# Kernel optimization log

Measured on AMD Instinct MI355X. Metric: run time of the kernel, lower is better.

## Reference

```python
import jax, jax.numpy as jnp
import numpy as np

N_NODES = 50000
HEADS = 4
NEG_SLOPE = 0.2


def _gat_conv(x, src, dst, W, a_src, a_dst, b):
    """PyG GATConv (concat=True, add_self_loops already applied to src/dst).
    x: [N, F_in], W: [F_in, H*C], a_src/a_dst: [H, C], b: [H*C]."""
    N = x.shape[0]
    HC = W.shape[1]
    C = HC // HEADS
    h = (x @ W).reshape(N, HEADS, C)                       # [N, H, C]
    alpha_s = (h * a_src[None]).sum(-1)                    # [N, H]
    alpha_d = (h * a_dst[None]).sum(-1)                    # [N, H]
    e = jax.nn.leaky_relu(alpha_s[src] + alpha_d[dst], NEG_SLOPE)  # [E, H]
    # segment softmax over incoming edges of each destination node
    m = jax.ops.segment_max(e, dst, num_segments=N)        # [N, H]
    ex = jnp.exp(e - m[dst])
    denom = jax.ops.segment_sum(ex, dst, num_segments=N)   # [N, H]
    alpha = ex / (denom[dst] + 1e-16)                      # [E, H]
    msg = h[src] * alpha[:, :, None]                       # [E, H, C]
    out = jax.ops.segment_sum(msg, dst, num_segments=N)    # [N, H, C]
    return out.reshape(N, HC) + b


def _glorot(key, shape, fan):
    lim = float(np.sqrt(6.0 / fan))
    return jax.random.uniform(key, shape, jnp.float32, -lim, lim)


def setup_inputs() -> dict:
    key = jax.random.key(0)
    ks = jax.random.split(key, 16)
    N, E, F_in, Hid, Out = N_NODES, 800000, 128, 256, 256
    x = jax.random.normal(ks[0], (N, F_in), jnp.float32)
    edge_index = jax.random.randint(ks[1], (2, E), 0, N, jnp.int64)
    C1, C2, C3 = Hid // HEADS, Hid // HEADS, Out // HEADS
    d = {"x": x, "edge_index": edge_index}
    dims = [(F_in, HEADS * C1, C1), (Hid, HEADS * C2, C2), (Hid, HEADS * C3, C3)]
    for i, (fi, fo, c) in enumerate(dims, 1):
        d[f"W{i}"] = _glorot(ks[3 * i], (fi, fo), fi + fo)
        d[f"a_src{i}"] = _glorot(ks[3 * i + 1], (HEADS, c), HEADS * c)
        d[f"a_dst{i}"] = _glorot(ks[3 * i + 2], (HEADS, c), HEADS * c)
        d[f"b{i}"] = jnp.zeros((fo,), jnp.float32)
    return d


def reference(x, edge_index, W1, a_src1, a_dst1, b1, W2, a_src2, a_dst2, b2, W3, a_src3, a_dst3, b3):
    N = x.shape[0]
    loops = jnp.arange(N, dtype=edge_index.dtype)
    src = jnp.concatenate([edge_index[0], loops])  # PyG add_self_loops=True
    dst = jnp.concatenate([edge_index[1], loops])
    h = _gat_conv(x, src, dst, W1, a_src1, a_dst1, b1)
    h = jax.nn.relu(h)  # dropout inert in eval mode
    h = _gat_conv(h, src, dst, W2, a_src2, a_dst2, b2)
    h = jax.nn.relu(h)
    return _gat_conv(h, src, dst, W3, a_src3, a_dst3, b3)
```

## Files before the change

kernel.cpp:

```cpp
#include <hip/hip_runtime.h>
#include <hip/hip_bf16.h>

typedef unsigned short u16;
typedef __attribute__((ext_vector_type(8))) short short8;
typedef __attribute__((ext_vector_type(4))) float f32x4;

#define HC 256
#define NHEAD 4

__device__ __forceinline__ u16 f2b_rne(float v) {
  __hip_bfloat16 b = __float2bfloat16(v);
  union { __hip_bfloat16 b; u16 u; } cv; cv.b = b; return cv.u;
}

__global__ void convert_w(const float* __restrict__ W, u16* __restrict__ Wth,
                          u16* __restrict__ Wtl, int K) {
  int id = blockIdx.x * 256 + threadIdx.x;
  if (id >= K * 256) return;
  int k = id >> 8, n = id & 255;
  float v = W[id];
  unsigned bits = __float_as_uint(v);
  u16 hi = (u16)(bits >> 16);
  float hf = __uint_as_float((unsigned)hi << 16);
  u16 lo = f2b_rne(v - hf);
  Wth[n * K + k] = hi;
  Wtl[n * K + k] = lo;
}

#define GBM 128
#define GBN 128
#define GBK 64

__global__ __launch_bounds__(256, 2) void gemm_mfma(
    const float* __restrict__ A, const u16* __restrict__ Bth,
    const u16* __restrict__ Btl, float* __restrict__ C,
    const float* __restrict__ a_src, const float* __restrict__ a_dst,
    float* __restrict__ AS, float* __restrict__ AD, int M, int K) {
  __shared__ u16 AH[128 * 64], AL[128 * 64], BH[128 * 64], BL[128 * 64];
  const int tid = threadIdx.x;
  const int lane = tid & 63;
  const int wave = tid >> 6;
  const int wm = (wave & 1) * 64;
  const int wn = (wave >> 1) * 64;
  const int bm = blockIdx.x * GBM;
  const int bn = blockIdx.y * GBN;

  const int srow = tid >> 1;
  const int skh  = (tid & 1) * 32;

  f32x4 acc[4][4] = {};

  const int agm = (bm + srow < M) ? (bm + srow) : (M - 1);

  for (int bk = 0; bk < K; bk += GBK) {
    float4 a0[4], a1[4];
    const float* arow = A + (size_t)agm * K + bk + skh;
#pragma unroll
    for (int u = 0; u < 4; ++u) {
      a0[u] = ((const float4*)arow)[2 * u];
      a1[u] = ((const float4*)arow)[2 * u + 1];
    }
    short8 sbh[4], sbl[4];
    const u16* bhrow = Bth + (size_t)(bn + srow) * K + bk + skh;
    const u16* blrow = Btl + (size_t)(bn + srow) * K + bk + skh;
#pragma unroll
    for (int u = 0; u < 4; ++u) {
      sbh[u] = *(const short8*)(bhrow + 8 * u);
      sbl[u] = *(const short8*)(blrow + 8 * u);
    }
    __syncthreads();
#pragma unroll
    for (int u = 0; u < 4; ++u) {
      int idx = (srow * 64 + skh + u * 8) ^ ((srow & 7) << 3);
      float va[8] = {a0[u].x, a0[u].y, a0[u].z, a0[u].w,
                     a1[u].x, a1[u].y, a1[u].z, a1[u].w};
      short8 hi, lo;
#pragma unroll
      for (int j = 0; j < 8; ++j) {
        unsigned bits = __float_as_uint(va[j]);
        u16 h = (u16)(bits >> 16);
        float hf = __uint_as_float((unsigned)h << 16);
        u16 l = f2b_rne(va[j] - hf);
        ((short*)&hi)[j] = (short)h;
        ((short*)&lo)[j] = (short)l;
      }
      *(short8*)&AH[idx] = hi;
      *(short8*)&AL[idx] = lo;
      *(short8*)&BH[idx] = sbh[u];
      *(short8*)&BL[idx] = sbl[u];
    }
    __syncthreads();
#pragma unroll
    for (int ks = 0; ks < 2; ++ks) {
      const int k0 = ks * 32 + (lane >> 4) * 8;
      short8 fah[4], fal[4], fbh[4], fbl[4];
#pragma unroll
      for (int mt = 0; mt < 4; ++mt) {
        int r = wm + mt * 16 + (lane & 15);
        int idx = (r * 64 + k0) ^ ((r & 7) << 3);
        fah[mt] = *(const short8*)&AH[idx];
        fal[mt] = *(const short8*)&AL[idx];
      }
#pragma unroll
      for (int nt = 0; nt < 4; ++nt) {
        int r = wn + nt * 16 + (lane & 15);
        int idx = (r * 64 + k0) ^ ((r & 7) << 3);
        fbh[nt] = *(const short8*)&BH[idx];
        fbl[nt] = *(const short8*)&BL[idx];
      }
#pragma unroll
      for (int mt = 0; mt < 4; ++mt)
#pragma unroll
        for (int nt = 0; nt < 4; ++nt) {
          acc[mt][nt] = __builtin_amdgcn_mfma_f32_16x16x32_bf16(
              fbh[nt], fah[mt], acc[mt][nt], 0, 0, 0);
          acc[mt][nt] = __builtin_amdgcn_mfma_f32_16x16x32_bf16(
              fbh[nt], fal[mt], acc[mt][nt], 0, 0, 0);
          acc[mt][nt] = __builtin_amdgcn_mfma_f32_16x16x32_bf16(
              fbl[nt], fah[mt], acc[mt][nt], 0, 0, 0);
        }
    }
  }
  const int headq = (bn + wn) >> 6;
  float4 sa[4], da[4];
#pragma unroll
  for (int nt = 0; nt < 4; ++nt) {
    sa[nt] = ((const float4*)a_src)[headq * 16 + nt * 4 + (lane >> 4)];
    da[nt] = ((const float4*)a_dst)[headq * 16 + nt * 4 + (lane >> 4)];
  }
#pragma unroll
  for (int mt = 0; mt < 4; ++mt) {
    const int row = bm + wm + mt * 16 + (lane & 15);
    float ps = 0.f, pd = 0.f;
#pragma unroll
    for (int nt = 0; nt < 4; ++nt) {
      ps += acc[mt][nt][0] * sa[nt].x + acc[mt][nt][1] * sa[nt].y +
            acc[mt][nt][2] * sa[nt].z + acc[mt][nt][3] * sa[nt].w;
      pd += acc[mt][nt][0] * da[nt].x + acc[mt][nt][1] * da[nt].y +
            acc[mt][nt][2] * da[nt].z + acc[mt][nt][3] * da[nt].w;
    }
    ps += __shfl_xor(ps, 16); ps += __shfl_xor(ps, 32);
    pd += __shfl_xor(pd, 16); pd += __shfl_xor(pd, 32);
    if (row < M) {
      float* cp = C + (size_t)row * HC + bn + wn + (lane >> 4) * 4;
#pragma unroll
      for (int nt = 0; nt < 4; ++nt)
        *(f32x4*)(cp + nt * 16) = acc[mt][nt];
      if ((lane >> 4) == 0) {
        AS[row * NHEAD + headq] = ps;
        AD[row * NHEAD + headq] = pd;
      }
    }
  }
}

__device__ __forceinline__ float comp4(float4 v, int i) {
  return (i == 0) ? v.x : (i == 1) ? v.y : (i == 2) ? v.z : v.w;
}

__global__ __launch_bounds__(256) void aggregate_kernel(
    const float* __restrict__ h, const float* __restrict__ as_g,
    const float* __restrict__ ad_g, const int* __restrict__ row_ptr,
    const int* __restrict__ csr_src, const float* __restrict__ bias,
    float* __restrict__ out, int relu_flag, int N) {
  const int wave = threadIdx.x >> 6;
  const int lane = threadIdx.x & 63;
  const int n = blockIdx.x * 4 + wave;
  if (n >= N) return;
  const int head = lane >> 4;
  const float4* __restrict__ h4 = (const float4*)h;
  const float4* __restrict__ as4 = (const float4*)as_g;

  const int beg = row_ptr[n];
  const int end = row_ptr[n + 1];

  float4 m4 = make_float4(-1e30f, -1e30f, -1e30f, -1e30f);
  for (int j = beg + lane; j < end; j += 64) {
    float4 a = as4[csr_src[j]];
    m4.x = fmaxf(m4.x, a.x); m4.y = fmaxf(m4.y, a.y);
    m4.z = fmaxf(m4.z, a.z); m4.w = fmaxf(m4.w, a.w);
  }
#pragma unroll
  for (int off = 32; off > 0; off >>= 1) {
    m4.x = fmaxf(m4.x, __shfl_xor(m4.x, off));
    m4.y = fmaxf(m4.y, __shfl_xor(m4.y, off));
    m4.z = fmaxf(m4.z, __shfl_xor(m4.z, off));
    m4.w = fmaxf(m4.w, __shfl_xor(m4.w, off));
  }
  const float ad = comp4(((const float4*)ad_g)[n], head);
  float mm = ad + comp4(m4, head);
  mm = (mm >= 0.f) ? mm : 0.2f * mm;

  float l = 0.f;
  float4 acc = make_float4(0.f, 0.f, 0.f, 0.f);
  for (int j0 = beg; j0 < end; j0 += 8) {
    int s[8];
    float ae[8];
    float4 hv[8];
#pragma unroll
    for (int u = 0; u < 8; ++u) {
      int j = j0 + u;
      s[u] = csr_src[(j < end) ? j : (end - 1)];
    }
#pragma unroll
    for (int u = 0; u < 8; ++u) ae[u] = as_g[s[u] * NHEAD + head];
#pragma unroll
    for (int u = 0; u < 8; ++u) hv[u] = h4[(size_t)s[u] * 64 + lane];
#pragma unroll
    for (int u = 0; u < 8; ++u) {
      float e = ae[u] + ad;
      e = (e >= 0.f) ? e : 0.2f * e;
      float p = __expf(e - mm);
      p = (j0 + u < end) ? p : 0.f;
      l += p;
      acc.x = fmaf(p, hv[u].x, acc.x);
      acc.y = fmaf(p, hv[u].y, acc.y);
      acc.z = fmaf(p, hv[u].z, acc.z);
      acc.w = fmaf(p, hv[u].w, acc.w);
    }
  }
  const float inv = 1.f / (l + 1e-16f);
  float4 b4 = ((const float4*)bias)[lane];
  float4 o;
  o.x = acc.x * inv + b4.x; o.y = acc.y * inv + b4.y;
  o.z = acc.z * inv + b4.z; o.w = acc.w * inv + b4.w;
  if (relu_flag) {
    o.x = fmaxf(o.x, 0.f); o.y = fmaxf(o.y, 0.f);
    o.z = fmaxf(o.z, 0.f); o.w = fmaxf(o.w, 0.f);
  }
  ((float4*)out)[(size_t)n * 64 + lane] = o;
}

__global__ void detect_kernel(const int* __restrict__ ei32, int* flag) {
  const int t = threadIdx.x;
  int bad = 0;
#pragma unroll
  for (int r = 0; r < 4; ++r) {
    int i = r * 64 + t;
    if (ei32[2 * i + 1] != 0) bad = 1;
  }
#pragma unroll
  for (int off = 32; off > 0; off >>= 1) bad |= __shfl_down(bad, off);
  if (t == 0) *flag = bad ? 0 : 1;
}

__device__ inline void edge_pair(const int* __restrict__ ei32,
                                 const long long* __restrict__ ei64, int is64,
                                 int e, int E, int& src, int& dst) {
  if (e < E) {
    if (is64) { src = (int)ei64[e]; dst = (int)ei64[(size_t)E + e]; }
    else      { src = ei32[e];      dst = ei32[(size_t)E + e]; }
  } else {
    src = dst = e - E;
  }
}

__global__ void count_kernel(const int* __restrict__ ei32, const int* __restrict__ flag,
                             int* __restrict__ cnt, int E, int Nn) {
  int e = blockIdx.x * blockDim.x + threadIdx.x;
  if (e >= E + Nn) return;
  int is64 = *flag;
  int src, dst;
  edge_pair(ei32, (const long long*)ei32, is64, e, E, src, dst);
  atomicAdd(&cnt[dst], 1);
}

__global__ void scatter_kernel(const int* __restrict__ ei32, const int* __restrict__ flag,
                               int* __restrict__ cursor, int* __restrict__ csr_src,
                               int E, int Nn) {
  int e = blockIdx.x * blockDim.x + threadIdx.x;
  if (e >= E + Nn) return;
  int is64 = *flag;
  int src, dst;
  edge_pair(ei32, (const long long*)ei32, is64, e, E, src, dst);
  int pos = atomicAdd(&cursor[dst], 1);
  csr_src[pos] = src;
}

__global__ __launch_bounds__(256) void scan_blocks(
    const int* __restrict__ cnt, int* __restrict__ local,
    int* __restrict__ partials, int Nn) {
  __shared__ int swave[4];
  const int t = threadIdx.x, lane = t & 63, w = t >> 6;
  const int idx = blockIdx.x * 256 + t;
  int v = (idx < Nn) ? cnt[idx] : 0;
  int x = v;
#pragma unroll
  for (int off = 1; off < 64; off <<= 1) {
    int y = __shfl_up(x, off);
    if (lane >= off) x += y;
  }
  if (lane == 63) swave[w] = x;
  __syncthreads();
  int wofs = 0;
#pragma unroll
  for (int i = 0; i < 3; ++i) wofs += (i < w) ? swave[i] : 0;
  if (idx < Nn) local[idx] = wofs + x - v;
  if (t == 255) partials[blockIdx.x] = wofs + x;
}

__global__ __launch_bounds__(256) void scan_partials(
    int* __restrict__ partials, int nb, int* __restrict__ total_out) {
  __shared__ int swave[4];
  const int t = threadIdx.x, lane = t & 63, w = t >> 6;
  int v = (t < nb) ? partials[t] : 0;
  int x = v;
#pragma unroll
  for (int off = 1; off < 64; off <<= 1) {
    int y = __shfl_up(x, off);
    if (lane >= off) x += y;
  }
  if (lane == 63) swave[w] = x;
  __syncthreads();
  int wofs = 0;
#pragma unroll
  for (int i = 0; i < 3; ++i) wofs += (i < w) ? swave[i] : 0;
  int excl = wofs + x - v;
  if (t < nb) partials[t] = excl;
  if (t == nb - 1) *total_out = excl + v;
}

__global__ void add_offsets(const int* __restrict__ local,
                            const int* __restrict__ partials,
                            int* __restrict__ row_ptr, int* __restrict__ cursor,
                            int Nn) {
  const int idx = blockIdx.x * 256 + threadIdx.x;
  if (idx < Nn) {
    int v = local[idx] + partials[blockIdx.x];
    row_ptr[idx] = v;
    cursor[idx] = v;
  }
}

static inline size_t align_up(size_t v) { return (v + 255) & ~(size_t)255; }

extern "C" void kernel_launch(void* const* d_in, const int* in_sizes, int n_in,
                              void* d_out, int out_size, void* d_ws, size_t ws_size,
                              hipStream_t stream) {
  const float* x      = (const float*)d_in[0];
  const int*   ei32   = (const int*)d_in[1];
  const float* W1     = (const float*)d_in[2];
  const float* asrc1  = (const float*)d_in[3];
  const float* adst1  = (const float*)d_in[4];
  const float* b1     = (const float*)d_in[5];
  const float* W2     = (const float*)d_in[6];
  const float* asrc2  = (const float*)d_in[7];
  const float* adst2  = (const float*)d_in[8];
  const float* b2     = (const float*)d_in[9];
  const float* W3     = (const float*)d_in[10];
  const float* asrc3  = (const float*)d_in[11];
  const float* adst3  = (const float*)d_in[12];
  const float* b3     = (const float*)d_in[13];

  const int N = in_sizes[0] / 128;
  const int E = in_sizes[1] / 2;
  const int ET = E + N;
  float* out = (float*)d_out;
  const int nb = (N + 255) / 256;

  char* w = (char*)d_ws;
  float* H       = (float*)w; w += align_up((size_t)N * HC * sizeof(float));
  float* AS      = (float*)w; w += align_up((size_t)N * NHEAD * sizeof(float));
  float* AD      = (float*)w; w += align_up((size_t)N * NHEAD * sizeof(float));
  int*   cnt     = (int*)w;   w += align_up((size_t)N * sizeof(int));
  int*   local   = (int*)w;   w += align_up((size_t)N * sizeof(int));
  int*   row_ptr = (int*)w;   w += align_up((size_t)(N + 1) * sizeof(int));
  int*   cursor  = (int*)w;   w += align_up((size_t)(N + 1) * sizeof(int));
  int*   parts   = (int*)w;   w += align_up(256 * sizeof(int));
  int*   csr_src = (int*)w;   w += align_up((size_t)ET * sizeof(int));
  u16*   Wth     = (u16*)w;   w += align_up((size_t)256 * 256 * sizeof(u16));
  u16*   Wtl     = (u16*)w;   w += align_up((size_t)256 * 256 * sizeof(u16));
  int*   flag    = (int*)w;   w += align_up(sizeof(int));

  hipMemsetAsync(cnt, 0, (size_t)N * sizeof(int), stream);
  detect_kernel<<<1, 64, 0, stream>>>(ei32, flag);
  count_kernel<<<(ET + 255) / 256, 256, 0, stream>>>(ei32, flag, cnt, E, N);
  scan_blocks<<<nb, 256, 0, stream>>>(cnt, local, parts, N);
  scan_partials<<<1, 256, 0, stream>>>(parts, nb, row_ptr + N);
  add_offsets<<<nb, 256, 0, stream>>>(local, parts, row_ptr, cursor, N);
  scatter_kernel<<<(ET + 255) / 256, 256, 0, stream>>>(ei32, flag, cursor, csr_src, E, N);

  const dim3 gemm_grid((N + GBM - 1) / GBM, HC / GBN);
  const int ablk = (N + 3) / 4;

  convert_w<<<(128 * 256 + 255) / 256, 256, 0, stream>>>(W1, Wth, Wtl, 128);
  gemm_mfma<<<gemm_grid, 256, 0, stream>>>(x, Wth, Wtl, H, asrc1, adst1, AS, AD, N, 128);
  aggregate_kernel<<<ablk, 256, 0, stream>>>(H, AS, AD, row_ptr, csr_src, b1, out, 1, N);

  convert_w<<<(256 * 256 + 255) / 256, 256, 0, stream>>>(W2, Wth, Wtl, 256);
  gemm_mfma<<<gemm_grid, 256, 0, stream>>>(out, Wth, Wtl, H, asrc2, adst2, AS, AD, N, 256);
  aggregate_kernel<<<ablk, 256, 0, stream>>>(H, AS, AD, row_ptr, csr_src, b2, out, 1, N);

  convert_w<<<(256 * 256 + 255) / 256, 256, 0, stream>>>(W3, Wth, Wtl, 256);
  gemm_mfma<<<gemm_grid, 256, 0, stream>>>(out, Wth, Wtl, H, asrc3, adst3, AS, AD, N, 256);
  aggregate_kernel<<<ablk, 256, 0, stream>>>(H, AS, AD, row_ptr, csr_src, b3, out, 0, N);
}
```

Before: 593.7 us.

## Split aggregation across two waves per node, swizzle GEMM blocks, batch weight conversion

The aggregate kernel now assigns two waves to each destination node. Each wave processes alternating 8-edge chunks, and the partial sums and normalisers are combined through shared memory, which doubles memory-level parallelism for the gather. The GEMM grid is flattened and remapped so both N-tiles of a group of 8 M-tiles run close together, improving reuse of A rows in L2. The three weight conversions are merged into one kernel launched up front with separate buffers, removing two launches. The cost is a block-wide sync in aggregation and extra redundant max-pass work per node.

```diff
diff --git a/kernel.cpp b/kernel.cpp
--- a/kernel.cpp
+++ b/kernel.cpp
@@ -13,18 +13,28 @@
   union { __hip_bfloat16 b; u16 u; } cv; cv.b = b; return cv.u;
 }
 
-__global__ void convert_w(const float* __restrict__ W, u16* __restrict__ Wth,
-                          u16* __restrict__ Wtl, int K) {
-  int id = blockIdx.x * 256 + threadIdx.x;
-  if (id >= K * 256) return;
-  int k = id >> 8, n = id & 255;
-  float v = W[id];
+__device__ __forceinline__ void w_split_store(const float* W, u16* Th, u16* Tl,
+                                              int K, int off) {
+  int k = off >> 8, n = off & 255;
+  float v = W[off];
   unsigned bits = __float_as_uint(v);
   u16 hi = (u16)(bits >> 16);
   float hf = __uint_as_float((unsigned)hi << 16);
   u16 lo = f2b_rne(v - hf);
-  Wth[n * K + k] = hi;
-  Wtl[n * K + k] = lo;
+  Th[n * K + k] = hi;
+  Tl[n * K + k] = lo;
+}
+
+__global__ void convert_w3(const float* __restrict__ W1, const float* __restrict__ W2,
+                           const float* __restrict__ W3,
+                           u16* __restrict__ Th1, u16* __restrict__ Tl1,
+                           u16* __restrict__ Th2, u16* __restrict__ Tl2,
+                           u16* __restrict__ Th3, u16* __restrict__ Tl3) {
+  int id = blockIdx.x * 256 + threadIdx.x;
+  const int S1 = 128 * 256, S2 = 256 * 256;
+  if (id < S1) w_split_store(W1, Th1, Tl1, 128, id);
+  else if (id < S1 + S2) w_split_store(W2, Th2, Tl2, 256, id - S1);
+  else if (id < S1 + 2 * S2) w_split_store(W3, Th3, Tl3, 256, id - S1 - S2);
 }
 
 #define GBM 128
@@ -35,15 +45,24 @@
     const float* __restrict__ A, const u16* __restrict__ Bth,
     const u16* __restrict__ Btl, float* __restrict__ C,
     const float* __restrict__ a_src, const float* __restrict__ a_dst,
-    float* __restrict__ AS, float* __restrict__ AD, int M, int K) {
+    float* __restrict__ AS, float* __restrict__ AD, int M, int K, int nMb) {
   __shared__ u16 AH[128 * 64], AL[128 * 64], BH[128 * 64], BL[128 * 64];
   const int tid = threadIdx.x;
   const int lane = tid & 63;
   const int wave = tid >> 6;
   const int wm = (wave & 1) * 64;
   const int wn = (wave >> 1) * 64;
-  const int bm = blockIdx.x * GBM;
-  const int bn = blockIdx.y * GBN;
+
+  const int bid = blockIdx.x;
+  const int g = bid >> 4;
+  const int r = bid & 15;
+  const int base = g * 8;
+  const int rem = nMb - base;
+  int bmi, bni;
+  if (rem >= 8) { bmi = base + (r & 7); bni = r >> 3; }
+  else          { bmi = base + (r % rem); bni = r / rem; }
+  const int bm = bmi * GBM;
+  const int bn = bni * GBN;
 
   const int srow = tid >> 1;
   const int skh  = (tid & 1) * 32;
@@ -96,15 +115,15 @@
       short8 fah[4], fal[4], fbh[4], fbl[4];
 #pragma unroll
       for (int mt = 0; mt < 4; ++mt) {
-        int r = wm + mt * 16 + (lane & 15);
-        int idx = (r * 64 + k0) ^ ((r & 7) << 3);
+        int rr = wm + mt * 16 + (lane & 15);
+        int idx = (rr * 64 + k0) ^ ((rr & 7) << 3);
         fah[mt] = *(const short8*)&AH[idx];
         fal[mt] = *(const short8*)&AL[idx];
       }
 #pragma unroll
       for (int nt = 0; nt < 4; ++nt) {
-        int r = wn + nt * 16 + (lane & 15);
-        int idx = (r * 64 + k0) ^ ((r & 7) << 3);
+        int rr = wn + nt * 16 + (lane & 15);
+        int idx = (rr * 64 + k0) ^ ((rr & 7) << 3);
         fbh[nt] = *(const short8*)&BH[idx];
         fbl[nt] = *(const short8*)&BL[idx];
       }
@@ -158,21 +177,25 @@
   return (i == 0) ? v.x : (i == 1) ? v.y : (i == 2) ? v.z : v.w;
 }
 
-__global__ __launch_bounds__(256) void aggregate_kernel(
+__global__ __launch_bounds__(512) void aggregate_kernel(
     const float* __restrict__ h, const float* __restrict__ as_g,
     const float* __restrict__ ad_g, const int* __restrict__ row_ptr,
     const int* __restrict__ csr_src, const float* __restrict__ bias,
     float* __restrict__ out, int relu_flag, int N) {
-  const int wave = threadIdx.x >> 6;
+  __shared__ float4 lacc[4][64];
+  __shared__ float lsum[4][64];
+  const int wid = threadIdx.x >> 6;
   const int lane = threadIdx.x & 63;
-  const int n = blockIdx.x * 4 + wave;
-  if (n >= N) return;
+  const int p = wid >> 1;
+  const int q = wid & 1;
+  const int n = blockIdx.x * 4 + p;
+  const int nc = (n < N) ? n : (N - 1);
   const int head = lane >> 4;
   const float4* __restrict__ h4 = (const float4*)h;
   const float4* __restrict__ as4 = (const float4*)as_g;
 
-  const int beg = row_ptr[n];
-  const int end = row_ptr[n + 1];
+  const int beg = row_ptr[nc];
+  const int end = row_ptr[nc + 1];
 
   float4 m4 = make_float4(-1e30f, -1e30f, -1e30f, -1e30f);
   for (int j = beg + lane; j < end; j += 64) {
@@ -187,13 +210,13 @@
     m4.z = fmaxf(m4.z, __shfl_xor(m4.z, off));
     m4.w = fmaxf(m4.w, __shfl_xor(m4.w, off));
   }
-  const float ad = comp4(((const float4*)ad_g)[n], head);
+  const float ad = comp4(((const float4*)ad_g)[nc], head);
   float mm = ad + comp4(m4, head);
   mm = (mm >= 0.f) ? mm : 0.2f * mm;
 
   float l = 0.f;
   float4 acc = make_float4(0.f, 0.f, 0.f, 0.f);
-  for (int j0 = beg; j0 < end; j0 += 8) {
+  for (int j0 = beg + q * 8; j0 < end; j0 += 16) {
     int s[8];
     float ae[8];
     float4 hv[8];
@@ -210,25 +233,32 @@
     for (int u = 0; u < 8; ++u) {
       float e = ae[u] + ad;
       e = (e >= 0.f) ? e : 0.2f * e;
-      float p = __expf(e - mm);
-      p = (j0 + u < end) ? p : 0.f;
-      l += p;
-      acc.x = fmaf(p, hv[u].x, acc.x);
-      acc.y = fmaf(p, hv[u].y, acc.y);
-      acc.z = fmaf(p, hv[u].z, acc.z);
-      acc.w = fmaf(p, hv[u].w, acc.w);
-    }
-  }
-  const float inv = 1.f / (l + 1e-16f);
-  float4 b4 = ((const float4*)bias)[lane];
-  float4 o;
-  o.x = acc.x * inv + b4.x; o.y = acc.y * inv + b4.y;
-  o.z = acc.z * inv + b4.z; o.w = acc.w * inv + b4.w;
-  if (relu_flag) {
-    o.x = fmaxf(o.x, 0.f); o.y = fmaxf(o.y, 0.f);
-    o.z = fmaxf(o.z, 0.f); o.w = fmaxf(o.w, 0.f);
-  }
-  ((float4*)out)[(size_t)n * 64 + lane] = o;
+      float pw = __expf(e - mm);
+      pw = (j0 + u < end) ? pw : 0.f;
+      l += pw;
+      acc.x = fmaf(pw, hv[u].x, acc.x);
+      acc.y = fmaf(pw, hv[u].y, acc.y);
+      acc.z = fmaf(pw, hv[u].z, acc.z);
+      acc.w = fmaf(pw, hv[u].w, acc.w);
+    }
+  }
+  if (q == 1) { lacc[p][lane] = acc; lsum[p][lane] = l; }
+  __syncthreads();
+  if (q == 0 && n < N) {
+    float4 a2 = lacc[p][lane];
+    acc.x += a2.x; acc.y += a2.y; acc.z += a2.z; acc.w += a2.w;
+    l += lsum[p][lane];
+    const float inv = 1.f / (l + 1e-16f);
+    float4 b4 = ((const float4*)bias)[lane];
+    float4 o;
+    o.x = acc.x * inv + b4.x; o.y = acc.y * inv + b4.y;
+    o.z = acc.z * inv + b4.z; o.w = acc.w * inv + b4.w;
+    if (relu_flag) {
+      o.x = fmaxf(o.x, 0.f); o.y = fmaxf(o.y, 0.f);
+      o.z = fmaxf(o.z, 0.f); o.w = fmaxf(o.w, 0.f);
+    }
+    ((float4*)out)[(size_t)n * 64 + lane] = o;
+  }
 }
 
 __global__ void detect_kernel(const int* __restrict__ ei32, int* flag) {
@@ -368,10 +398,16 @@
   int*   cursor  = (int*)w;   w += align_up((size_t)(N + 1) * sizeof(int));
   int*   parts   = (int*)w;   w += align_up(256 * sizeof(int));
   int*   csr_src = (int*)w;   w += align_up((size_t)ET * sizeof(int));
-  u16*   Wth     = (u16*)w;   w += align_up((size_t)256 * 256 * sizeof(u16));
-  u16*   Wtl     = (u16*)w;   w += align_up((size_t)256 * 256 * sizeof(u16));
+  u16*   Wth1    = (u16*)w;   w += align_up((size_t)128 * 256 * sizeof(u16));
+  u16*   Wtl1    = (u16*)w;   w += align_up((size_t)128 * 256 * sizeof(u16));
+  u16*   Wth2    = (u16*)w;   w += align_up((size_t)256 * 256 * sizeof(u16));
+  u16*   Wtl2    = (u16*)w;   w += align_up((size_t)256 * 256 * sizeof(u16));
+  u16*   Wth3    = (u16*)w;   w += align_up((size_t)256 * 256 * sizeof(u16));
+  u16*   Wtl3    = (u16*)w;   w += align_up((size_t)256 * 256 * sizeof(u16));
   int*   flag    = (int*)w;   w += align_up(sizeof(int));
 
+  convert_w3<<<(128 * 256 + 2 * 256 * 256 + 255) / 256, 256, 0, stream>>>(
+      W1, W2, W3, Wth1, Wtl1, Wth2, Wtl2, Wth3, Wtl3);
   hipMemsetAsync(cnt, 0, (size_t)N * sizeof(int), stream);
   detect_kernel<<<1, 64, 0, stream>>>(ei32, flag);
   count_kernel<<<(ET + 255) / 256, 256, 0, stream>>>(ei32, flag, cnt, E, N);
@@ -380,18 +416,16 @@
   add_offsets<<<nb, 256, 0, stream>>>(local, parts, row_ptr, cursor, N);
   scatter_kernel<<<(ET + 255) / 256, 256, 0, stream>>>(ei32, flag, cursor, csr_src, E, N);
 
-  const dim3 gemm_grid((N + GBM - 1) / GBM, HC / GBN);
+  const int nMb = (N + GBM - 1) / GBM;
+  const int gemm_blocks = nMb * 2;
   const int ablk = (N + 3) / 4;
 
-  convert_w<<<(128 * 256 + 255) / 256, 256, 0, stream>>>(W1, Wth, Wtl, 128);
-  gemm_mfma<<<gemm_grid, 256, 0, stream>>>(x, Wth, Wtl, H, asrc1, adst1, AS, AD, N, 128);
-  aggregate_kernel<<<ablk, 256, 0, stream>>>(H, AS, AD, row_ptr, csr_src, b1, out, 1, N);
-
-  convert_w<<<(256 * 256 + 255) / 256, 256, 0, stream>>>(W2, Wth, Wtl, 256);
-  gemm_mfma<<<gemm_grid, 256, 0, stream>>>(out, Wth, Wtl, H, asrc2, adst2, AS, AD, N, 256);
-  aggregate_kernel<<<ablk, 256, 0, stream>>>(H, AS, AD, row_ptr, csr_src, b2, out, 1, N);
-
-  convert_w<<<(256 * 256 + 255) / 256, 256, 0, stream>>>(W3, Wth, Wtl, 256);
-  gemm_mfma<<<gemm_grid, 256, 0, stream>>>(out, Wth, Wtl, H, asrc3, adst3, AS, AD, N, 256);
-  aggregate_kernel<<<ablk, 256, 0, stream>>>(H, AS, AD, row_ptr, csr_src, b3, out, 0, N);
-}
+  gemm_mfma<<<gemm_blocks, 256, 0, stream>>>(x, Wth1, Wtl1, H, asrc1, adst1, AS, AD, N, 128, nMb);
+  aggregate_kernel<<<ablk, 512, 0, stream>>>(H, AS, AD, row_ptr, csr_src, b1, out, 1, N);
+
+  gemm_mfma<<<gemm_blocks, 256, 0, stream>>>(out, Wth2, Wtl2, H, asrc2, adst2, AS, AD, N, 256, nMb);
+  aggregate_kernel<<<ablk, 512, 0, stream>>>(H, AS, AD, row_ptr, csr_src, b2, out, 1, N);
+
+  gemm_mfma<<<gemm_blocks, 256, 0, stream>>>(out, Wth3, Wtl3, H, asrc3, adst3, AS, AD, N, 256, nMb);
+  aggregate_kernel<<<ablk, 512, 0, stream>>>(H, AS, AD, row_ptr, csr_src, b3, out, 0, N);
+}
```

After: 598.4 us. No clear change (+0.8%).
